# Optimization experiments

Hardware: AMD Instinct MI355X
Metric: run time of the kernel (lower is better)

Reference implementation:

```python
import math
import jax, jax.numpy as jnp
import numpy as np

T = 2048       # sequence_length
H = 2048       # hidden_size
NH = 32        # num_attention_heads
NKV = 8        # num_key_value_heads
HD = 64        # head_dim
SW = 128       # sliding_window
QM = NH // NKV # q_mult (GQA group size)
ROPE_THETA = 10000.0
EPS = 1e-5


def setup_inputs() -> dict:
    key = jax.random.key(0)
    k_x, k_s, k_qkv, k_out = jax.random.split(key, 4)
    x = jax.random.normal(k_x, (T, H), dtype=jnp.float32)
    scale = jnp.ones((H,), dtype=jnp.float32)
    sinks = jax.random.normal(k_s, (NH,), dtype=jnp.float32) * 0.02
    qkv_dim = HD * (NH + 2 * NKV)  # 3072
    qkv_kernel = jax.random.normal(k_qkv, (H, qkv_dim), dtype=jnp.float32) * (1.0 / math.sqrt(H))
    qkv_bias = jnp.zeros((qkv_dim,), dtype=jnp.float32)
    out_kernel = jax.random.normal(k_out, (H, H), dtype=jnp.float32) * (1.0 / math.sqrt(H))
    out_bias = jnp.zeros((H,), dtype=jnp.float32)
    # RoPE tables: [T, HD//2]
    half = HD // 2
    inv_freq = 1.0 / (ROPE_THETA ** (np.arange(half, dtype=np.float64) / half))
    ang = np.outer(np.arange(T, dtype=np.float64), inv_freq)
    cos_table = jnp.asarray(np.cos(ang), dtype=jnp.float32)
    sin_table = jnp.asarray(np.sin(ang), dtype=jnp.float32)
    # causal + sliding-window additive mask [T, T]
    qp = np.arange(T, dtype=np.int32)[:, None]
    kp = np.arange(T, dtype=np.int32)[None, :]
    m = np.where(kp > qp, -np.inf, 0.0) + np.where(qp - kp > SW, -np.inf, 0.0)
    mask = jnp.asarray(m, dtype=jnp.float32)
    return dict(x=x, scale=scale, sinks=sinks, qkv_kernel=qkv_kernel,
                qkv_bias=qkv_bias, out_kernel=out_kernel, out_bias=out_bias,
                cos_table=cos_table, sin_table=sin_table, mask=mask)


def _rmsnorm(x, scale):
    t = x.astype(jnp.float32)
    rms = jnp.sqrt(jnp.mean(t * t, axis=-1, keepdims=True) + EPS)
    return ((t / rms) * scale).astype(x.dtype)


def _rope(x, cos, sin):
    # x: [T, ..., HD]; split-half rotation as in the reference RotaryEmbedding
    shp = x.shape
    xr = x.reshape(shp[0], -1, HD)
    c = cos[:, None, :].astype(xr.dtype)
    s = sin[:, None, :].astype(xr.dtype)
    x1, x2 = jnp.split(xr, 2, axis=-1)
    y = jnp.concatenate([x1 * c - x2 * s, x2 * c + x1 * s], axis=-1)
    return y.reshape(shp)


def reference(x, scale, sinks, qkv_kernel, qkv_bias, out_kernel, out_bias,
              cos_table, sin_table, mask):
    normed = _rmsnorm(x, scale)
    qkv = normed @ qkv_kernel + qkv_bias                 # [T, 3072]
    q_end = NH * HD
    k_end = q_end + NKV * HD
    q = qkv[:, :q_end].reshape(T, NKV, QM, HD)           # [T, nkv, qm, hd]
    k = qkv[:, q_end:k_end].reshape(T, NKV, HD)          # [T, nkv, hd]
    v = qkv[:, k_end:].reshape(T, NKV, HD)               # [T, nkv, hd]
    q = _rope(q, cos_table, sin_table)
    k = _rope(k, cos_table, sin_table)
    sm_scale = 1.0 / math.sqrt(float(HD))
    # GQA attention without materializing repeated K/V
    logits = jnp.einsum('qnmd,knd->nmqk', q, k) * sm_scale  # [nkv, qm, T, T]
    logits = logits + mask[None, None, :, :]
    sink_col = jnp.broadcast_to(sinks.reshape(NKV, QM, 1, 1), (NKV, QM, T, 1))
    logits = jnp.concatenate([logits, sink_col], axis=-1)   # [nkv, qm, T, T+1]
    weights = jax.nn.softmax(logits, axis=-1)[..., :-1]     # drop sink column
    attn = jnp.einsum('nmqk,knd->qnmd', weights, v).reshape(T, NH * HD)
    projected = attn @ out_kernel + out_bias
    return x + projected
```

## Files before the change

kernel.cpp:

```cpp
#include <hip/hip_runtime.h>
#include <hip/hip_bf16.h>
#include <stdint.h>

typedef __bf16 bf16_t;
typedef __attribute__((ext_vector_type(8))) __bf16 bf16x8;
typedef __attribute__((ext_vector_type(4))) __bf16 bf16x4;
typedef __attribute__((ext_vector_type(4))) float f32x4;

static constexpr int T_SEQ = 2048;
static constexpr int HID   = 2048;
static constexpr int NHEAD = 32;
static constexpr int NKVH  = 8;
static constexpr int HDIM  = 64;
static constexpr int QKVD  = 3072;

__device__ inline f32x4 mfma16(bf16x8 a, bf16x8 b, f32x4 c) {
    return __builtin_amdgcn_mfma_f32_16x16x32_bf16(a, b, c, 0, 0, 0);
}

__device__ inline void load_lds16(const bf16_t* g, bf16_t* l) {
    __builtin_amdgcn_global_load_lds(
        (const __attribute__((address_space(1))) void*)g,
        (__attribute__((address_space(3))) void*)l, 16, 0, 0);
}

__global__ __launch_bounds__(256) void prep_kernel(const float* __restrict__ Wq,
                                                   const float* __restrict__ Wo,
                                                   bf16_t* __restrict__ Tq,
                                                   bf16_t* __restrict__ To,
                                                   const float* __restrict__ x,
                                                   const float* __restrict__ scale,
                                                   bf16_t* __restrict__ normed) {
    __shared__ float tile[64 * 65];
    int b = blockIdx.x;
    const int t = threadIdx.x;
    if (b < 2560) {
        const float* in; bf16_t* outw; int NN, KK, bx, by;
        if (b < 1536) { in = Wq; outw = Tq; NN = QKVD; KK = HID; bx = b % 48; by = b / 48; }
        else { b -= 1536; in = Wo; outw = To; NN = HID; KK = HID; bx = b % 32; by = b / 32; }
        const int c4 = (t & 15) * 4;
#pragma unroll
        for (int i = 0; i < 4; ++i) {
            int r = (t >> 4) + i * 16;
            float4 v = *(const float4*)(in + (size_t)(by*64 + r) * NN + bx*64 + c4);
            tile[r*65 + c4 + 0] = v.x; tile[r*65 + c4 + 1] = v.y;
            tile[r*65 + c4 + 2] = v.z; tile[r*65 + c4 + 3] = v.w;
        }
        __syncthreads();
        const int kc = t & 7;
#pragma unroll
        for (int i = 0; i < 2; ++i) {
            int n = (t >> 3) + i * 32;
            bf16x8 o;
#pragma unroll
            for (int j = 0; j < 8; ++j) o[j] = (bf16_t)tile[(kc*8 + j)*65 + n];
            *(bf16x8*)(outw + (size_t)(bx*64 + n) * KK + by*64 + kc*8) = o;
        }
    } else {
        int row = b - 2560;
        const float4* x4 = (const float4*)(x + (size_t)row * HID);
        const float4* s4 = (const float4*)scale;
        float4 v0 = x4[t], v1 = x4[t + 256];
        float ss = v0.x*v0.x + v0.y*v0.y + v0.z*v0.z + v0.w*v0.w
                 + v1.x*v1.x + v1.y*v1.y + v1.z*v1.z + v1.w*v1.w;
#pragma unroll
        for (int off = 32; off > 0; off >>= 1) ss += __shfl_down(ss, off);
        if ((t & 63) == 0) tile[t >> 6] = ss;
        __syncthreads();
        float total = tile[0] + tile[1] + tile[2] + tile[3];
        float inv = rsqrtf(total * (1.0f / HID) + 1e-5f);
        float4 sc0 = s4[t], sc1 = s4[t + 256];
        bf16_t* outr = normed + (size_t)row * HID;
        bf16x4 o0, o1;
        o0.x = (bf16_t)(v0.x*inv*sc0.x); o0.y = (bf16_t)(v0.y*inv*sc0.y);
        o0.z = (bf16_t)(v0.z*inv*sc0.z); o0.w = (bf16_t)(v0.w*inv*sc0.w);
        o1.x = (bf16_t)(v1.x*inv*sc1.x); o1.y = (bf16_t)(v1.y*inv*sc1.y);
        o1.z = (bf16_t)(v1.z*inv*sc1.z); o1.w = (bf16_t)(v1.w*inv*sc1.w);
        *(bf16x4*)(outr + 4*t)        = o0;
        *(bf16x4*)(outr + 1024 + 4*t) = o1;
    }
}

__global__ __launch_bounds__(256) void gemm_qkv_rope(const bf16_t* __restrict__ A,
                                                     const bf16_t* __restrict__ Bt,
                                                     const float* __restrict__ qkvb,
                                                     const float* __restrict__ cost,
                                                     const float* __restrict__ sint,
                                                     bf16_t* __restrict__ Qb,
                                                     bf16_t* __restrict__ Kb,
                                                     bf16_t* __restrict__ Vb) {
    __shared__ __align__(16) bf16_t Asm[2 * 128 * 32];
    __shared__ __align__(16) bf16_t Bsm[2 * 128 * 32];
    const int K = HID;
    const int tid = threadIdx.x;
    const int bm = blockIdx.y * 128, bn = blockIdx.x * 128;
    const int lane = tid & 63, wave = tid >> 6;
    const int wm = (wave & 1) * 64, wn = (wave >> 1) * 64;
    const int lm = lane & 15, quad = lane >> 4;

    f32x4 acc[4][4];
#pragma unroll
    for (int i = 0; i < 4; ++i)
#pragma unroll
        for (int j = 0; j < 4; ++j) acc[i][j] = (f32x4){0.f, 0.f, 0.f, 0.f};

    const int cid0 = tid, cid1 = tid + 256;
    const int r0 = cid0 >> 2, c0 = (cid0 & 3) ^ ((r0 >> 1) & 3);
    const int r1 = cid1 >> 2, c1 = (cid1 & 3) ^ ((r1 >> 1) & 3);
    const bf16_t* Ab = A  + (size_t)bm * K;
    const bf16_t* Bb = Bt + (size_t)bn * K;
    const size_t ga0 = (size_t)r0 * K + c0 * 8;
    const size_t ga1 = (size_t)r1 * K + c1 * 8;
    bf16_t* ldsA0a = &Asm[wave * 512];
    bf16_t* ldsA0b = &Asm[2048 + wave * 512];
    bf16_t* ldsA1a = &Asm[4096 + wave * 512];
    bf16_t* ldsA1b = &Asm[4096 + 2048 + wave * 512];
    bf16_t* ldsB0a = &Bsm[wave * 512];
    bf16_t* ldsB0b = &Bsm[2048 + wave * 512];
    bf16_t* ldsB1a = &Bsm[4096 + wave * 512];
    bf16_t* ldsB1b = &Bsm[4096 + 2048 + wave * 512];
    const int swz = (quad ^ ((lm >> 1) & 3)) * 8;

    for (int k0 = 0; k0 < K; k0 += 64) {
        load_lds16(Ab + ga0 + k0,      ldsA0a);
        load_lds16(Ab + ga1 + k0,      ldsA0b);
        load_lds16(Ab + ga0 + k0 + 32, ldsA1a);
        load_lds16(Ab + ga1 + k0 + 32, ldsA1b);
        load_lds16(Bb + ga0 + k0,      ldsB0a);
        load_lds16(Bb + ga1 + k0,      ldsB0b);
        load_lds16(Bb + ga0 + k0 + 32, ldsB1a);
        load_lds16(Bb + ga1 + k0 + 32, ldsB1b);
        __syncthreads();
#pragma unroll
        for (int ks = 0; ks < 2; ++ks) {
            bf16x8 af[4], bfr[4];
#pragma unroll
            for (int i = 0; i < 4; ++i)
                af[i]  = *(const bf16x8*)&Asm[ks*4096 + (wm + i*16 + lm)*32 + swz];
#pragma unroll
            for (int j = 0; j < 4; ++j)
                bfr[j] = *(const bf16x8*)&Bsm[ks*4096 + (wn + j*16 + lm)*32 + swz];
#pragma unroll
            for (int i = 0; i < 4; ++i)
#pragma unroll
                for (int j = 0; j < 4; ++j) acc[i][j] = mfma16(af[i], bfr[j], acc[i][j]);
        }
        __syncthreads();
    }

    const int gcb = bn + wn;
    bf16_t* dstbase; int cstride, coff; bool dorope;
    if (bn < 2048)      { dstbase = Qb; cstride = 2048; coff = 0;    dorope = true;  }
    else if (bn < 2560) { dstbase = Kb; cstride = 512;  coff = 2048; dorope = true;  }
    else                { dstbase = Vb; cstride = 512;  coff = 2560; dorope = false; }
    float bj[4];
#pragma unroll
    for (int j = 0; j < 4; ++j) bj[j] = qkvb[gcb + j*16 + lm];
    const int colb = gcb - coff + lm;

#pragma unroll
    for (int i = 0; i < 4; ++i) {
        const int tr = bm + wm + i*16 + quad*4;
#pragma unroll
        for (int r = 0; r < 4; ++r) {
            const int t = tr + r;
            bf16_t* drow = dstbase + (size_t)t * cstride + colb;
            if (dorope) {
                float c0 = cost[t*32 + lm],      s0 = sint[t*32 + lm];
                float c1 = cost[t*32 + 16 + lm], s1 = sint[t*32 + 16 + lm];
                float x10 = acc[i][0][r] + bj[0], x20 = acc[i][2][r] + bj[2];
                float x11 = acc[i][1][r] + bj[1], x21 = acc[i][3][r] + bj[3];
                drow[0]  = (bf16_t)(x10*c0 - x20*s0);
                drow[16] = (bf16_t)(x11*c1 - x21*s1);
                drow[32] = (bf16_t)(x20*c0 + x10*s0);
                drow[48] = (bf16_t)(x21*c1 + x11*s1);
            } else {
                drow[0]  = (bf16_t)(acc[i][0][r] + bj[0]);
                drow[16] = (bf16_t)(acc[i][1][r] + bj[1]);
                drow[32] = (bf16_t)(acc[i][2][r] + bj[2]);
                drow[48] = (bf16_t)(acc[i][3][r] + bj[3]);
            }
        }
    }
}

__global__ __launch_bounds__(256) void gemm_splitk(const bf16_t* __restrict__ A,
                                                   const bf16_t* __restrict__ Bt,
                                                   bf16_t* __restrict__ Cpart,
                                                   int M, int N, int K) {
    __shared__ __align__(16) bf16_t Asm[2 * 128 * 32];
    __shared__ __align__(16) bf16_t Bsm[2 * 128 * 32];
    const int tid = threadIdx.x;
    const int bm = blockIdx.y * 128, bn = blockIdx.x * 128;
    const int kh = K >> 1;
    const int kb = blockIdx.z * kh;
    const int lane = tid & 63, wave = tid >> 6;
    const int wm = (wave & 1) * 64, wn = (wave >> 1) * 64;
    const int lm = lane & 15, quad = lane >> 4;

    f32x4 acc[4][4];
#pragma unroll
    for (int i = 0; i < 4; ++i)
#pragma unroll
        for (int j = 0; j < 4; ++j) acc[i][j] = (f32x4){0.f, 0.f, 0.f, 0.f};

    const int cid0 = tid, cid1 = tid + 256;
    const int r0 = cid0 >> 2, c0 = (cid0 & 3) ^ ((r0 >> 1) & 3);
    const int r1 = cid1 >> 2, c1 = (cid1 & 3) ^ ((r1 >> 1) & 3);
    const bf16_t* Ab = A  + (size_t)bm * K + kb;
    const bf16_t* Bb = Bt + (size_t)bn * K + kb;
    const size_t ga0 = (size_t)r0 * K + c0 * 8;
    const size_t ga1 = (size_t)r1 * K + c1 * 8;
    bf16_t* ldsA0a = &Asm[wave * 512];
    bf16_t* ldsA0b = &Asm[2048 + wave * 512];
    bf16_t* ldsA1a = &Asm[4096 + wave * 512];
    bf16_t* ldsA1b = &Asm[4096 + 2048 + wave * 512];
    bf16_t* ldsB0a = &Bsm[wave * 512];
    bf16_t* ldsB0b = &Bsm[2048 + wave * 512];
    bf16_t* ldsB1a = &Bsm[4096 + wave * 512];
    bf16_t* ldsB1b = &Bsm[4096 + 2048 + wave * 512];
    const int swz = (quad ^ ((lm >> 1) & 3)) * 8;

    for (int k0 = 0; k0 < kh; k0 += 64) {
        load_lds16(Ab + ga0 + k0,      ldsA0a);
        load_lds16(Ab + ga1 + k0,      ldsA0b);
        load_lds16(Ab + ga0 + k0 + 32, ldsA1a);
        load_lds16(Ab + ga1 + k0 + 32, ldsA1b);
        load_lds16(Bb + ga0 + k0,      ldsB0a);
        load_lds16(Bb + ga1 + k0,      ldsB0b);
        load_lds16(Bb + ga0 + k0 + 32, ldsB1a);
        load_lds16(Bb + ga1 + k0 + 32, ldsB1b);
        __syncthreads();
#pragma unroll
        for (int ks = 0; ks < 2; ++ks) {
            bf16x8 af[4], bfr[4];
#pragma unroll
            for (int i = 0; i < 4; ++i)
                af[i]  = *(const bf16x8*)&Asm[ks*4096 + (wm + i*16 + lm)*32 + swz];
#pragma unroll
            for (int j = 0; j < 4; ++j)
                bfr[j] = *(const bf16x8*)&Bsm[ks*4096 + (wn + j*16 + lm)*32 + swz];
#pragma unroll
            for (int i = 0; i < 4; ++i)
#pragma unroll
                for (int j = 0; j < 4; ++j) acc[i][j] = mfma16(af[i], bfr[j], acc[i][j]);
        }
        __syncthreads();
    }

    bf16_t* Cp = Cpart + (size_t)blockIdx.z * M * N;
#pragma unroll
    for (int i = 0; i < 4; ++i) {
        int gr = bm + wm + i*16 + quad*4;
#pragma unroll
        for (int j = 0; j < 4; ++j) {
            int gc = bn + wn + j*16 + lm;
#pragma unroll
            for (int r = 0; r < 4; ++r)
                Cp[(size_t)(gr + r)*N + gc] = (bf16_t)acc[i][j][r];
        }
    }
}

__global__ __launch_bounds__(256) void combine_out(const bf16_t* __restrict__ p0,
                                                   const bf16_t* __restrict__ p1,
                                                   const float* __restrict__ bias,
                                                   const float* __restrict__ x,
                                                   float* __restrict__ out) {
    const int n4 = T_SEQ * HID / 4;
    for (int i4 = blockIdx.x * 256 + threadIdx.x; i4 < n4; i4 += gridDim.x * 256) {
        bf16x4 a = *(const bf16x4*)(p0 + (size_t)i4 * 4);
        bf16x4 b = *(const bf16x4*)(p1 + (size_t)i4 * 4);
        float4 xv = *(const float4*)(x + (size_t)i4 * 4);
        int col4 = (i4 * 4) & (HID - 1);
        float4 bi = *(const float4*)(bias + col4);
        float4 o;
        o.x = (float)a.x + (float)b.x + bi.x + xv.x;
        o.y = (float)a.y + (float)b.y + bi.y + xv.y;
        o.z = (float)a.z + (float)b.z + bi.z + xv.z;
        o.w = (float)a.w + (float)b.w + bi.w + xv.w;
        *(float4*)(out + (size_t)i4 * 4) = o;
    }
}

__global__ __launch_bounds__(256) void attn_kernel(const bf16_t* __restrict__ Qb,
                                                   const bf16_t* __restrict__ Kb,
                                                   const bf16_t* __restrict__ Vb,
                                                   const float* __restrict__ sinks,
                                                   bf16_t* __restrict__ attnb) {
    __shared__ __align__(16) bf16_t Vt[64 * 200];
    __shared__ __align__(16) bf16_t Ws[64 * 200];

    const int tid = threadIdx.x;
    const int qt = blockIdx.x, h = blockIdx.y;
    const int qs = qt * 64;
    const int nkv = h >> 2;

    {
        const int off = (tid >> 5) * 8;
#pragma unroll
        for (int it = 0; it < 3; ++it) {
            int j2 = (tid & 31) + 32 * it;
            int kg0 = qs - 128 + 2*j2;     if (kg0 < 0) kg0 = 0;
            int kg1 = qs - 128 + 2*j2 + 1; if (kg1 < 0) kg1 = 0;
            union { uint4 u; bf16_t e[8]; } v0, v1;
            v0.u = *(const uint4*)(Vb + ((size_t)kg0*NKVH + nkv)*HDIM + off);
            v1.u = *(const uint4*)(Vb + ((size_t)kg1*NKVH + nkv)*HDIM + off);
#pragma unroll
            for (int r = 0; r < 8; ++r) {
                union { uint u; bf16_t e[2]; } p;
                p.e[0] = v0.e[r]; p.e[1] = v1.e[r];
                *(uint*)&Vt[(off + r)*200 + 2*j2] = p.u;
            }
        }
    }

    const int lane = tid & 63, wave = tid >> 6;
    const int lm = lane & 15, quad = lane >> 4;
    const int w16 = wave * 16;

    f32x4 S[12];
#pragma unroll
    for (int jt = 0; jt < 12; ++jt) S[jt] = (f32x4){0.f, 0.f, 0.f, 0.f};
    const bf16_t* Qrow = Qb + ((size_t)(qs + w16 + lm)*NHEAD + h)*HDIM + quad*8;
    int krow[12];
#pragma unroll
    for (int jt = 0; jt < 12; ++jt) {
        int kg = qs - 128 + jt*16 + lm;
        krow[jt] = kg < 0 ? 0 : kg;
    }
    __builtin_amdgcn_s_setprio(1);
#pragma unroll
    for (int ks = 0; ks < 2; ++ks) {
        bf16x8 aq = *(const bf16x8*)(Qrow + ks*32);
#pragma unroll
        for (int jt = 0; jt < 12; ++jt) {
            bf16x8 bk = *(const bf16x8*)(Kb + ((size_t)krow[jt]*NKVH + nkv)*HDIM + ks*32 + quad*8);
            S[jt] = mfma16(aq, bk, S[jt]);
        }
    }
    __builtin_amdgcn_s_setprio(0);

    const float sink = sinks[h];
#pragma unroll
    for (int reg = 0; reg < 4; ++reg) {
        const int qg = qs + w16 + quad*4 + reg;
        float mx = -1e30f;
#pragma unroll
        for (int jt = 0; jt < 12; ++jt) {
            int kg = qs - 128 + jt*16 + lm;
            float sv = S[jt][reg] * 0.125f;
            bool valid = (kg >= 0) && (kg <= qg) && (qg - kg <= 128);
            sv = valid ? sv : -1e30f;
            S[jt][reg] = sv;
            mx = fmaxf(mx, sv);
        }
#pragma unroll
        for (int off = 1; off < 16; off <<= 1) mx = fmaxf(mx, __shfl_xor(mx, off));
        float M = fmaxf(mx, sink);
        float sum = 0.f;
#pragma unroll
        for (int jt = 0; jt < 12; ++jt) {
            float e = __expf(S[jt][reg] - M);
            S[jt][reg] = e; sum += e;
        }
#pragma unroll
        for (int off = 1; off < 16; off <<= 1) sum += __shfl_xor(sum, off);
        float rden = 1.f / (sum + __expf(sink - M));
#pragma unroll
        for (int jt = 0; jt < 12; ++jt)
            Ws[(w16 + quad*4 + reg)*200 + jt*16 + lm] = (bf16_t)(S[jt][reg] * rden);
    }
    __syncthreads();

    f32x4 O[4];
#pragma unroll
    for (int nt = 0; nt < 4; ++nt) O[nt] = (f32x4){0.f, 0.f, 0.f, 0.f};
    __builtin_amdgcn_s_setprio(1);
#pragma unroll
    for (int ks = 0; ks < 6; ++ks) {
        bf16x8 aw = *(const bf16x8*)&Ws[(w16 + lm)*200 + ks*32 + quad*8];
#pragma unroll
        for (int nt = 0; nt < 4; ++nt) {
            bf16x8 bv = *(const bf16x8*)&Vt[(nt*16 + lm)*200 + ks*32 + quad*8];
            O[nt] = mfma16(aw, bv, O[nt]);
        }
    }
    __builtin_amdgcn_s_setprio(0);
#pragma unroll
    for (int nt = 0; nt < 4; ++nt)
#pragma unroll
        for (int reg = 0; reg < 4; ++reg)
            attnb[(size_t)(qs + w16 + quad*4 + reg)*HID + h*HDIM + nt*16 + lm] =
                (bf16_t)(O[nt][reg]);
}

extern "C" void kernel_launch(void* const* d_in, const int* in_sizes, int n_in,
                              void* d_out, int out_size, void* d_ws, size_t ws_size,
                              hipStream_t stream) {
    (void)in_sizes; (void)n_in; (void)out_size; (void)ws_size;
    const float* x          = (const float*)d_in[0];
    const float* scale      = (const float*)d_in[1];
    const float* sinks      = (const float*)d_in[2];
    const float* qkv_kernel = (const float*)d_in[3];
    const float* qkv_bias   = (const float*)d_in[4];
    const float* out_kernel = (const float*)d_in[5];
    const float* out_bias   = (const float*)d_in[6];
    const float* cos_t      = (const float*)d_in[7];
    const float* sin_t      = (const float*)d_in[8];
    float* out = (float*)d_out;

    char* ws = (char*)d_ws;
    const size_t MiB = 1048576;
    bf16_t* Wt_out = (bf16_t*)(ws);
    bf16_t* Wt_qkv = (bf16_t*)(ws + 8*MiB);
    bf16_t* attnb  = (bf16_t*)(ws + 8*MiB);
    bf16_t* normed = (bf16_t*)(ws + 20*MiB);
    bf16_t* Qb     = (bf16_t*)(ws + 28*MiB);
    bf16_t* Kb     = (bf16_t*)(ws + 36*MiB);
    bf16_t* Vb     = (bf16_t*)(ws + 38*MiB);
    bf16_t* outp   = (bf16_t*)(ws + 40*MiB);

    prep_kernel<<<4608, 256, 0, stream>>>(qkv_kernel, out_kernel, Wt_qkv, Wt_out,
                                          x, scale, normed);
    gemm_qkv_rope<<<dim3(QKVD/128, T_SEQ/128), 256, 0, stream>>>(normed, Wt_qkv,
                                                                 qkv_bias, cos_t, sin_t,
                                                                 Qb, Kb, Vb);
    attn_kernel<<<dim3(T_SEQ/64, NHEAD), 256, 0, stream>>>(Qb, Kb, Vb, sinks, attnb);
    gemm_splitk<<<dim3(HID/128, T_SEQ/128, 2), 256, 0, stream>>>(attnb, Wt_out, outp,
                                                                 T_SEQ, HID, HID);
    combine_out<<<2048, 256, 0, stream>>>(outp, outp + (size_t)T_SEQ*HID, out_bias, x, out);
}
```

Baseline: 220.2 us.

## Use 64x128 GEMM tiles and fuse output projection with bias and residual

Both GEMMs now share a 64x128 tile core macro, which doubles the block count for the QKV GEMM. The output projection drops split-K and the separate combine kernel, and writes bias plus residual directly from the accumulators in fp32. This removes the bf16 partial-sum round trip and one kernel launch, and avoids rounding the partials to bf16. In exchange, each output block runs the full K loop, and the smaller M tile lowers operand reuse per block.

```diff
diff --git a/kernel.cpp b/kernel.cpp
--- a/kernel.cpp
+++ b/kernel.cpp
@@ -81,6 +81,60 @@
     }
 }
 
+#define GEMM64_CORE(Aptr, Btptr, Kdim)                                          \
+    __shared__ __align__(16) bf16_t Asm[2 * 64 * 32];                 \
+    __shared__ __align__(16) bf16_t Bsm[2 * 128 * 32];               \
+    const int K = (Kdim);                                                       \
+    const int tid = threadIdx.x;                                                \
+    const int bm = blockIdx.y * 64, bn = blockIdx.x * 128;                      \
+    const int lane = tid & 63, wave = tid >> 6;                                 \
+    const int wm = (wave & 1) * 32, wn = (wave >> 1) * 64;                      \
+    const int lm = lane & 15, quad = lane >> 4;                                 \
+    f32x4 acc[2][4];                                                            \
+    _Pragma("unroll")                                                           \
+    for (int i = 0; i < 2; ++i)                                                 \
+        _Pragma("unroll")                                                       \
+        for (int j = 0; j < 4; ++j) acc[i][j] = (f32x4){0.f, 0.f, 0.f, 0.f};    \
+    const int r0 = tid >> 2, c0 = (tid & 3) ^ ((r0 >> 1) & 3);                  \
+    const int cid1 = tid + 256;                                                 \
+    const int r1 = cid1 >> 2, c1 = (cid1 & 3) ^ ((r1 >> 1) & 3);                \
+    const bf16_t* Ab = (Aptr) + (size_t)bm * K;                                 \
+    const bf16_t* Bb = (Btptr) + (size_t)bn * K;                                \
+    const size_t gaA  = (size_t)r0 * K + c0 * 8;                                \
+    const size_t gaB0 = (size_t)r0 * K + c0 * 8;                                \
+    const size_t gaB1 = (size_t)r1 * K + c1 * 8;                                \
+    bf16_t* ldsA0  = &Asm[wave * 512];                                          \
+    bf16_t* ldsA1  = &Asm[2048 + wave * 512];                                   \
+    bf16_t* ldsB0a = &Bsm[wave * 512];                                          \
+    bf16_t* ldsB0b = &Bsm[2048 + wave * 512];                                   \
+    bf16_t* ldsB1a = &Bsm[4096 + wave * 512];                                   \
+    bf16_t* ldsB1b = &Bsm[4096 + 2048 + wave * 512];                            \
+    const int swz = (quad ^ ((lm >> 1) & 3)) * 8;                               \
+    for (int k0 = 0; k0 < K; k0 += 64) {                                        \
+        load_lds16(Ab + gaA  + k0,      ldsA0);                                 \
+        load_lds16(Ab + gaA  + k0 + 32, ldsA1);                                 \
+        load_lds16(Bb + gaB0 + k0,      ldsB0a);                                \
+        load_lds16(Bb + gaB1 + k0,      ldsB0b);                                \
+        load_lds16(Bb + gaB0 + k0 + 32, ldsB1a);                                \
+        load_lds16(Bb + gaB1 + k0 + 32, ldsB1b);                                \
+        __syncthreads();                                                        \
+        _Pragma("unroll")                                                       \
+        for (int ks = 0; ks < 2; ++ks) {                                        \
+            bf16x8 af[2], bfr[4];                                               \
+            _Pragma("unroll")                                                   \
+            for (int i = 0; i < 2; ++i)                                         \
+                af[i]  = *(const bf16x8*)&Asm[ks*2048 + (wm + i*16 + lm)*32 + swz]; \
+            _Pragma("unroll")                                                   \
+            for (int j = 0; j < 4; ++j)                                         \
+                bfr[j] = *(const bf16x8*)&Bsm[ks*4096 + (wn + j*16 + lm)*32 + swz]; \
+            _Pragma("unroll")                                                   \
+            for (int i = 0; i < 2; ++i)                                         \
+                _Pragma("unroll")                                               \
+                for (int j = 0; j < 4; ++j) acc[i][j] = mfma16(af[i], bfr[j], acc[i][j]); \
+        }                                                                       \
+        __syncthreads();                                                        \
+    }
+
 __global__ __launch_bounds__(256) void gemm_qkv_rope(const bf16_t* __restrict__ A,
                                                      const bf16_t* __restrict__ Bt,
                                                      const float* __restrict__ qkvb,
@@ -89,64 +143,7 @@
                                                      bf16_t* __restrict__ Qb,
                                                      bf16_t* __restrict__ Kb,
                                                      bf16_t* __restrict__ Vb) {
-    __shared__ __align__(16) bf16_t Asm[2 * 128 * 32];
-    __shared__ __align__(16) bf16_t Bsm[2 * 128 * 32];
-    const int K = HID;
-    const int tid = threadIdx.x;
-    const int bm = blockIdx.y * 128, bn = blockIdx.x * 128;
-    const int lane = tid & 63, wave = tid >> 6;
-    const int wm = (wave & 1) * 64, wn = (wave >> 1) * 64;
-    const int lm = lane & 15, quad = lane >> 4;
-
-    f32x4 acc[4][4];
-#pragma unroll
-    for (int i = 0; i < 4; ++i)
-#pragma unroll
-        for (int j = 0; j < 4; ++j) acc[i][j] = (f32x4){0.f, 0.f, 0.f, 0.f};
-
-    const int cid0 = tid, cid1 = tid + 256;
-    const int r0 = cid0 >> 2, c0 = (cid0 & 3) ^ ((r0 >> 1) & 3);
-    const int r1 = cid1 >> 2, c1 = (cid1 & 3) ^ ((r1 >> 1) & 3);
-    const bf16_t* Ab = A  + (size_t)bm * K;
-    const bf16_t* Bb = Bt + (size_t)bn * K;
-    const size_t ga0 = (size_t)r0 * K + c0 * 8;
-    const size_t ga1 = (size_t)r1 * K + c1 * 8;
-    bf16_t* ldsA0a = &Asm[wave * 512];
-    bf16_t* ldsA0b = &Asm[2048 + wave * 512];
-    bf16_t* ldsA1a = &Asm[4096 + wave * 512];
-    bf16_t* ldsA1b = &Asm[4096 + 2048 + wave * 512];
-    bf16_t* ldsB0a = &Bsm[wave * 512];
-    bf16_t* ldsB0b = &Bsm[2048 + wave * 512];
-    bf16_t* ldsB1a = &Bsm[4096 + wave * 512];
-    bf16_t* ldsB1b = &Bsm[4096 + 2048 + wave * 512];
-    const int swz = (quad ^ ((lm >> 1) & 3)) * 8;
-
-    for (int k0 = 0; k0 < K; k0 += 64) {
-        load_lds16(Ab + ga0 + k0,      ldsA0a);
-        load_lds16(Ab + ga1 + k0,      ldsA0b);
-        load_lds16(Ab + ga0 + k0 + 32, ldsA1a);
-        load_lds16(Ab + ga1 + k0 + 32, ldsA1b);
-        load_lds16(Bb + ga0 + k0,      ldsB0a);
-        load_lds16(Bb + ga1 + k0,      ldsB0b);
-        load_lds16(Bb + ga0 + k0 + 32, ldsB1a);
-        load_lds16(Bb + ga1 + k0 + 32, ldsB1b);
-        __syncthreads();
-#pragma unroll
-        for (int ks = 0; ks < 2; ++ks) {
-            bf16x8 af[4], bfr[4];
-#pragma unroll
-            for (int i = 0; i < 4; ++i)
-                af[i]  = *(const bf16x8*)&Asm[ks*4096 + (wm + i*16 + lm)*32 + swz];
-#pragma unroll
-            for (int j = 0; j < 4; ++j)
-                bfr[j] = *(const bf16x8*)&Bsm[ks*4096 + (wn + j*16 + lm)*32 + swz];
-#pragma unroll
-            for (int i = 0; i < 4; ++i)
-#pragma unroll
-                for (int j = 0; j < 4; ++j) acc[i][j] = mfma16(af[i], bfr[j], acc[i][j]);
-        }
-        __syncthreads();
-    }
+    GEMM64_CORE(A, Bt, HID)
 
     const int gcb = bn + wn;
     bf16_t* dstbase; int cstride, coff; bool dorope;
@@ -159,7 +156,7 @@
     const int colb = gcb - coff + lm;
 
 #pragma unroll
-    for (int i = 0; i < 4; ++i) {
+    for (int i = 0; i < 2; ++i) {
         const int tr = bm + wm + i*16 + quad*4;
 #pragma unroll
         for (int r = 0; r < 4; ++r) {
@@ -184,102 +181,32 @@
     }
 }
 
-__global__ __launch_bounds__(256) void gemm_splitk(const bf16_t* __restrict__ A,
-                                                   const bf16_t* __restrict__ Bt,
-                                                   bf16_t* __restrict__ Cpart,
-                                                   int M, int N, int K) {
-    __shared__ __align__(16) bf16_t Asm[2 * 128 * 32];
-    __shared__ __align__(16) bf16_t Bsm[2 * 128 * 32];
-    const int tid = threadIdx.x;
-    const int bm = blockIdx.y * 128, bn = blockIdx.x * 128;
-    const int kh = K >> 1;
-    const int kb = blockIdx.z * kh;
-    const int lane = tid & 63, wave = tid >> 6;
-    const int wm = (wave & 1) * 64, wn = (wave >> 1) * 64;
-    const int lm = lane & 15, quad = lane >> 4;
-
-    f32x4 acc[4][4];
-#pragma unroll
-    for (int i = 0; i < 4; ++i)
-#pragma unroll
-        for (int j = 0; j < 4; ++j) acc[i][j] = (f32x4){0.f, 0.f, 0.f, 0.f};
-
-    const int cid0 = tid, cid1 = tid + 256;
-    const int r0 = cid0 >> 2, c0 = (cid0 & 3) ^ ((r0 >> 1) & 3);
-    const int r1 = cid1 >> 2, c1 = (cid1 & 3) ^ ((r1 >> 1) & 3);
-    const bf16_t* Ab = A  + (size_t)bm * K + kb;
-    const bf16_t* Bb = Bt + (size_t)bn * K + kb;
-    const size_t ga0 = (size_t)r0 * K + c0 * 8;
-    const size_t ga1 = (size_t)r1 * K + c1 * 8;
-    bf16_t* ldsA0a = &Asm[wave * 512];
-    bf16_t* ldsA0b = &Asm[2048 + wave * 512];
-    bf16_t* ldsA1a = &Asm[4096 + wave * 512];
-    bf16_t* ldsA1b = &Asm[4096 + 2048 + wave * 512];
-    bf16_t* ldsB0a = &Bsm[wave * 512];
-    bf16_t* ldsB0b = &Bsm[2048 + wave * 512];
-    bf16_t* ldsB1a = &Bsm[4096 + wave * 512];
-    bf16_t* ldsB1b = &Bsm[4096 + 2048 + wave * 512];
-    const int swz = (quad ^ ((lm >> 1) & 3)) * 8;
-
-    for (int k0 = 0; k0 < kh; k0 += 64) {
-        load_lds16(Ab + ga0 + k0,      ldsA0a);
-        load_lds16(Ab + ga1 + k0,      ldsA0b);
-        load_lds16(Ab + ga0 + k0 + 32, ldsA1a);
-        load_lds16(Ab + ga1 + k0 + 32, ldsA1b);
-        load_lds16(Bb + ga0 + k0,      ldsB0a);
-        load_lds16(Bb + ga1 + k0,      ldsB0b);
-        load_lds16(Bb + ga0 + k0 + 32, ldsB1a);
-        load_lds16(Bb + ga1 + k0 + 32, ldsB1b);
-        __syncthreads();
-#pragma unroll
-        for (int ks = 0; ks < 2; ++ks) {
-            bf16x8 af[4], bfr[4];
-#pragma unroll
-            for (int i = 0; i < 4; ++i)
-                af[i]  = *(const bf16x8*)&Asm[ks*4096 + (wm + i*16 + lm)*32 + swz];
-#pragma unroll
-            for (int j = 0; j < 4; ++j)
-                bfr[j] = *(const bf16x8*)&Bsm[ks*4096 + (wn + j*16 + lm)*32 + swz];
-#pragma unroll
-            for (int i = 0; i < 4; ++i)
-#pragma unroll
-                for (int j = 0; j < 4; ++j) acc[i][j] = mfma16(af[i], bfr[j], acc[i][j]);
-        }
-        __syncthreads();
-    }
-
-    bf16_t* Cp = Cpart + (size_t)blockIdx.z * M * N;
-#pragma unroll
-    for (int i = 0; i < 4; ++i) {
-        int gr = bm + wm + i*16 + quad*4;
-#pragma unroll
-        for (int j = 0; j < 4; ++j) {
-            int gc = bn + wn + j*16 + lm;
-#pragma unroll
-            for (int r = 0; r < 4; ++r)
-                Cp[(size_t)(gr + r)*N + gc] = (bf16_t)acc[i][j][r];
-        }
-    }
-}
-
-__global__ __launch_bounds__(256) void combine_out(const bf16_t* __restrict__ p0,
-                                                   const bf16_t* __restrict__ p1,
-                                                   const float* __restrict__ bias,
-                                                   const float* __restrict__ x,
-                                                   float* __restrict__ out) {
-    const int n4 = T_SEQ * HID / 4;
-    for (int i4 = blockIdx.x * 256 + threadIdx.x; i4 < n4; i4 += gridDim.x * 256) {
-        bf16x4 a = *(const bf16x4*)(p0 + (size_t)i4 * 4);
-        bf16x4 b = *(const bf16x4*)(p1 + (size_t)i4 * 4);
-        float4 xv = *(const float4*)(x + (size_t)i4 * 4);
-        int col4 = (i4 * 4) & (HID - 1);
-        float4 bi = *(const float4*)(bias + col4);
-        float4 o;
-        o.x = (float)a.x + (float)b.x + bi.x + xv.x;
-        o.y = (float)a.y + (float)b.y + bi.y + xv.y;
-        o.z = (float)a.z + (float)b.z + bi.z + xv.z;
-        o.w = (float)a.w + (float)b.w + bi.w + xv.w;
-        *(float4*)(out + (size_t)i4 * 4) = o;
+__global__ __launch_bounds__(256) void gemm_out_res(const bf16_t* __restrict__ A,
+                                                    const bf16_t* __restrict__ Bt,
+                                                    const float* __restrict__ bias,
+                                                    const float* __restrict__ x,
+                                                    float* __restrict__ out) {
+    GEMM64_CORE(A, Bt, HID)
+
+    const int gcb = bn + wn;
+    float bj[4];
+#pragma unroll
+    for (int j = 0; j < 4; ++j) bj[j] = bias[gcb + j*16 + lm];
+
+#pragma unroll
+    for (int i = 0; i < 2; ++i) {
+        const int tr = bm + wm + i*16 + quad*4;
+#pragma unroll
+        for (int r = 0; r < 4; ++r) {
+            const int t = tr + r;
+            const float* xrow = x + (size_t)t * HID;
+            float* orow = out + (size_t)t * HID;
+#pragma unroll
+            for (int j = 0; j < 4; ++j) {
+                const int gc = gcb + j*16 + lm;
+                orow[gc] = acc[i][j][r] + bj[j] + xrow[gc];
+            }
+        }
     }
 }
 
@@ -419,15 +346,13 @@
     bf16_t* Qb     = (bf16_t*)(ws + 28*MiB);
     bf16_t* Kb     = (bf16_t*)(ws + 36*MiB);
     bf16_t* Vb     = (bf16_t*)(ws + 38*MiB);
-    bf16_t* outp   = (bf16_t*)(ws + 40*MiB);
 
     prep_kernel<<<4608, 256, 0, stream>>>(qkv_kernel, out_kernel, Wt_qkv, Wt_out,
                                           x, scale, normed);
-    gemm_qkv_rope<<<dim3(QKVD/128, T_SEQ/128), 256, 0, stream>>>(normed, Wt_qkv,
-                                                                 qkv_bias, cos_t, sin_t,
-                                                                 Qb, Kb, Vb);
+    gemm_qkv_rope<<<dim3(QKVD/128, T_SEQ/64), 256, 0, stream>>>(normed, Wt_qkv,
+                                                                qkv_bias, cos_t, sin_t,
+                                                                Qb, Kb, Vb);
     attn_kernel<<<dim3(T_SEQ/64, NHEAD), 256, 0, stream>>>(Qb, Kb, Vb, sinks, attnb);
-    gemm_splitk<<<dim3(HID/128, T_SEQ/128, 2), 256, 0, stream>>>(attnb, Wt_out, outp,
-                                                                 T_SEQ, HID, HID);
-    combine_out<<<2048, 256, 0, stream>>>(outp, outp + (size_t)T_SEQ*HID, out_bias, x, out);
-}
+    gemm_out_res<<<dim3(HID/128, T_SEQ/64), 256, 0, stream>>>(attnb, Wt_out,
+                                                              out_bias, x, out);
+}
```

Result: faster. 205.8 us (-6.5%).
